# Optimization experiments

Hardware: AMD Instinct MI355X
Metric: run time of the kernel (lower is better)

The kernel has to match this reference:

```python
import jax, jax.numpy as jnp
import numpy as np

RADIUS = 0.2
NSAMPLE = 32
USE_XYZ = True

B, N, S, C = 8, 8192, 2048, 64


def setup_inputs() -> dict:
    key = jax.random.key(0)
    k1, k2, k3 = jax.random.split(key, 3)
    xyz = jax.random.uniform(k1, (B, N, 3), dtype=jnp.float32)
    new_xyz = jax.random.uniform(k2, (B, S, 3), dtype=jnp.float32)
    features = jax.random.normal(k3, (B, N, C), dtype=jnp.float32)
    return {"xyz": xyz, "new_xyz": new_xyz, "features": features}


def _ball_query(new_xyz, xyz, radius, nsample):
    # new_xyz: (B,S,3), xyz: (B,N,3) -> idx (B,S,nsample) int32
    n = xyz.shape[1]
    d2 = jnp.sum((new_xyz[:, :, None, :] - xyz[:, None, :, :]) ** 2, axis=-1)  # (B,S,N)
    mask = d2 < radius * radius
    # keys: index j if inside ball else N (sentinel); smallest nsample keys = first
    # nsample in-ball indices in ascending j order (matches CUDA ball_query order).
    keys = jnp.where(mask, jnp.arange(n, dtype=jnp.int32), jnp.int32(n))
    neg_vals, _ = jax.lax.top_k(-keys, nsample)  # top_k of -keys -> smallest keys
    idx = -neg_vals  # (B,S,nsample), ascending
    first = idx[..., 0:1]
    idx = jnp.where(idx == n, first, idx)   # pad empty slots with first hit
    idx = jnp.where(idx == n, 0, idx)       # balls with zero hits -> index 0
    return idx


def _group(points, idx):
    # points: (B,N,D), idx: (B,S,K) -> (B,S,K,D)
    return jax.vmap(lambda p, i: p[i])(points, idx)


def reference(xyz, new_xyz, features):
    idx = _ball_query(new_xyz, xyz, RADIUS, NSAMPLE)
    grouped_xyz = _group(xyz, idx) - new_xyz[:, :, None, :]  # (B,S,K,3)
    grouped_feat = _group(features, idx)                      # (B,S,K,C)
    if USE_XYZ:
        new_features = jnp.concatenate([grouped_xyz, grouped_feat], axis=-1)
    else:
        new_features = grouped_feat
    return jnp.transpose(new_features, (0, 3, 1, 2))  # (B, C+3, S, K)
```

## Files before the change

### kernel.cpp

```cpp
#include <hip/hip_runtime.h>

#define BB 8
#define NN 8192
#define SS 2048
#define CC 64
#define NS 32
#define COUT 67
#define QT 8
#define SLOTS (QT*NS)
#define SP 260

__global__ __launch_bounds__(256, 6) void fused_kernel(
    const float* __restrict__ xyz,
    const float* __restrict__ new_xyz,
    const float* __restrict__ feat,
    float* __restrict__ out)
{
#pragma clang fp contract(off)
    __shared__ float fh[16 * SP];
    __shared__ float xt[3 * SP];
    __shared__ int idx_sh[SLOTS];

    const int t   = threadIdx.x;
    const int w   = t >> 6;
    const int ln  = t & 63;
    const int bid = blockIdx.x;
    const int b     = bid & 7;
    const int sTile = bid >> 3;
    const int s0 = sTile * QT;

    for (int qi = 0; qi < 2; ++qi) {
        const int q = (qi << 2) + w;
        const int s = s0 + q;
        const float R2 = 0.04f;

        const float* ctr = new_xyz + ((size_t)b * SS + s) * 3;
        const float cx = ctr[0], cy = ctr[1], cz = ctr[2];
        const float* xb = xyz + (size_t)b * NN * 3;

        int* myidx = idx_sh + (q << 5);
        const unsigned long long lt = (1ull << ln) - 1ull;

        int total = 0;
        int firstIdx = -1;
        for (int j0 = 0; j0 < NN && total < NS; j0 += 256) {
            const float4* p4 = (const float4*)(xb + (size_t)(j0 + (ln << 2)) * 3);
            const float4 A  = p4[0];
            const float4 Bv = p4[1];
            const float4 Cv = p4[2];
            float d2v[4];
            {
                const float dx = A.x - cx, dy = A.y - cy, dz = A.z - cz;
                float d2 = dx * dx; d2 = d2 + dy * dy; d2 = d2 + dz * dz;
                d2v[0] = d2;
            }
            {
                const float dx = A.w - cx, dy = Bv.x - cy, dz = Bv.y - cz;
                float d2 = dx * dx; d2 = d2 + dy * dy; d2 = d2 + dz * dz;
                d2v[1] = d2;
            }
            {
                const float dx = Bv.z - cx, dy = Bv.w - cy, dz = Cv.x - cz;
                float d2 = dx * dx; d2 = d2 + dy * dy; d2 = d2 + dz * dz;
                d2v[2] = d2;
            }
            {
                const float dx = Cv.y - cx, dy = Cv.z - cy, dz = Cv.w - cz;
                float d2 = dx * dx; d2 = d2 + dy * dy; d2 = d2 + dz * dz;
                d2v[3] = d2;
            }

            unsigned long long M[4];
#pragma unroll
            for (int u = 0; u < 4; ++u) M[u] = __ballot(d2v[u] < R2);

            if (firstIdx < 0) {
                int fmin = 0x7fffffff;
#pragma unroll
                for (int u = 0; u < 4; ++u)
                    if (M[u] != 0ull) {
                        const int j = j0 + (__builtin_ctzll(M[u]) << 2) + u;
                        fmin = (j < fmin) ? j : fmin;
                    }
                if (fmin != 0x7fffffff) firstIdx = fmin;
            }

            int below = 0;
#pragma unroll
            for (int u = 0; u < 4; ++u) below += (int)__popcll(M[u] & lt);

            int own = 0;
#pragma unroll
            for (int u = 0; u < 4; ++u) {
                if (d2v[u] < R2) {
                    const int pos = total + below + own;
                    if (pos < NS) myidx[pos] = j0 + (ln << 2) + u;
                    ++own;
                }
            }
#pragma unroll
            for (int u = 0; u < 4; ++u) total += (int)__popcll(M[u]);
        }
        if (total < NS) {
            const int fill = (total > 0) ? firstIdx : 0;
            if (ln >= total && ln < NS) myidx[ln] = fill;
        }
    }
    __syncthreads();

    const int c4  = ln & 3;
    const int ms  = ln >> 2;
    const float* fb = feat + (size_t)b * NN * CC;
    const size_t plane = (size_t)SS * NS;
    float* ob = out + ((size_t)b * COUT * SS + s0) * NS;

    {
        const int r = idx_sh[t];
        const int q = t >> 5;
        const float* ctr = new_xyz + ((size_t)b * SS + s0 + q) * 3;
        const float* p   = xyz + ((size_t)b * NN + r) * 3;
        xt[0 * SP + t] = p[0] - ctr[0];
        xt[1 * SP + t] = p[1] - ctr[1];
        xt[2 * SP + t] = p[2] - ctr[2];
    }

#pragma unroll
    for (int st = 0; st < 4; ++st) {
        if (st > 0) __syncthreads();

        float4 vv[4];
        int    mm[4];
#pragma unroll
        for (int i = 0; i < 4; ++i) {
            mm[i] = (w << 6) + (i << 4) + ms;
            vv[i] = *(const float4*)(fb + (size_t)idx_sh[mm[i]] * CC
                                     + (st << 4) + (c4 << 2));
        }
#pragma unroll
        for (int i = 0; i < 4; ++i) {
            fh[((c4 << 2) + 0) * SP + mm[i]] = vv[i].x;
            fh[((c4 << 2) + 1) * SP + mm[i]] = vv[i].y;
            fh[((c4 << 2) + 2) * SP + mm[i]] = vv[i].z;
            fh[((c4 << 2) + 3) * SP + mm[i]] = vv[i].w;
        }
        __syncthreads();

        if (st == 0) {
            for (int i = 0; i < 5; ++i) {
                const int tau = (i << 2) + w;
                if (tau < 19) {
                    const float* src = (tau < 3) ? (xt + tau * SP)
                                                 : (fh + (tau - 3) * SP);
                    const float4 v = *(const float4*)(src + (ln << 2));
                    *(float4*)(ob + (size_t)tau * plane + (ln << 2)) = v;
                }
            }
        } else {
#pragma unroll
            for (int i = 0; i < 4; ++i) {
                const int tau = (i << 2) + w;
                const float4 v = *(const float4*)(fh + tau * SP + (ln << 2));
                *(float4*)(ob + (size_t)(3 + (st << 4) + tau) * plane
                           + (ln << 2)) = v;
            }
        }
    }
}

extern "C" void kernel_launch(void* const* d_in, const int* in_sizes, int n_in,
                              void* d_out, int out_size, void* d_ws, size_t ws_size,
                              hipStream_t stream) {
    const float* xyz     = (const float*)d_in[0];
    const float* new_xyz = (const float*)d_in[1];
    const float* feat    = (const float*)d_in[2];
    float* out = (float*)d_out;
    (void)d_ws; (void)ws_size;

    fused_kernel<<<dim3((BB * SS) / QT), dim3(256), 0, stream>>>(xyz, new_xyz, feat, out);
}
```

Measured before the change: 175.5 us.

## Software-pipeline feature gather in 8-channel stages with smaller shared tile

The feature gather now moves 8 channels per stage over 8 stages instead of 16 channels over 4. The next stage's global loads are issued before the barrier, so they overlap with the current stage's shared-to-global stores. The shared feature buffer is halved, and launch bounds now ask for 8 blocks per CU to raise occupancy. The cost is twice as many barriers and stages, each global load now fetching only 32 bytes per row (two lanes per gather row instead of four), and tighter register limits.

Result: no change. 177.0 us (+0.8%).

```diff
diff --git a/kernel.cpp b/kernel.cpp
--- a/kernel.cpp
+++ b/kernel.cpp
@@ -10,14 +10,14 @@
 #define SLOTS (QT*NS)
 #define SP 260
 
-__global__ __launch_bounds__(256, 6) void fused_kernel(
+__global__ __launch_bounds__(256, 8) void fused_kernel(
     const float* __restrict__ xyz,
     const float* __restrict__ new_xyz,
     const float* __restrict__ feat,
     float* __restrict__ out)
 {
 #pragma clang fp contract(off)
-    __shared__ float fh[16 * SP];
+    __shared__ float fh[8 * SP];
     __shared__ float xt[3 * SP];
     __shared__ int idx_sh[SLOTS];
 
@@ -108,8 +108,8 @@
     }
     __syncthreads();
 
-    const int c4  = ln & 3;
-    const int ms  = ln >> 2;
+    const int c2 = ln & 1;
+    const int ms = ln >> 1;
     const float* fb = feat + (size_t)b * NN * CC;
     const size_t plane = (size_t)SS * NS;
     float* ob = out + ((size_t)b * COUT * SS + s0) * NS;
@@ -124,31 +124,35 @@
         xt[2 * SP + t] = p[2] - ctr[2];
     }
 
+    const int m0 = (w << 6) + ms;
+    const int m1 = m0 + 32;
+    const float* rp0 = fb + (size_t)idx_sh[m0] * CC + (c2 << 2);
+    const float* rp1 = fb + (size_t)idx_sh[m1] * CC + (c2 << 2);
+
+    float4 v0 = *(const float4*)(rp0);
+    float4 v1 = *(const float4*)(rp1);
+
 #pragma unroll
-    for (int st = 0; st < 4; ++st) {
-        if (st > 0) __syncthreads();
+    for (int st = 0; st < 8; ++st) {
+        fh[((c2 << 2) + 0) * SP + m0] = v0.x;
+        fh[((c2 << 2) + 1) * SP + m0] = v0.y;
+        fh[((c2 << 2) + 2) * SP + m0] = v0.z;
+        fh[((c2 << 2) + 3) * SP + m0] = v0.w;
+        fh[((c2 << 2) + 0) * SP + m1] = v1.x;
+        fh[((c2 << 2) + 1) * SP + m1] = v1.y;
+        fh[((c2 << 2) + 2) * SP + m1] = v1.z;
+        fh[((c2 << 2) + 3) * SP + m1] = v1.w;
 
-        float4 vv[4];
-        int    mm[4];
-#pragma unroll
-        for (int i = 0; i < 4; ++i) {
-            mm[i] = (w << 6) + (i << 4) + ms;
-            vv[i] = *(const float4*)(fb + (size_t)idx_sh[mm[i]] * CC
-                                     + (st << 4) + (c4 << 2));
-        }
-#pragma unroll
-        for (int i = 0; i < 4; ++i) {
-            fh[((c4 << 2) + 0) * SP + mm[i]] = vv[i].x;
-            fh[((c4 << 2) + 1) * SP + mm[i]] = vv[i].y;
-            fh[((c4 << 2) + 2) * SP + mm[i]] = vv[i].z;
-            fh[((c4 << 2) + 3) * SP + mm[i]] = vv[i].w;
+        if (st < 7) {
+            v0 = *(const float4*)(rp0 + ((st + 1) << 3));
+            v1 = *(const float4*)(rp1 + ((st + 1) << 3));
         }
         __syncthreads();
 
         if (st == 0) {
-            for (int i = 0; i < 5; ++i) {
+            for (int i = 0; i < 3; ++i) {
                 const int tau = (i << 2) + w;
-                if (tau < 19) {
+                if (tau < 11) {
                     const float* src = (tau < 3) ? (xt + tau * SP)
                                                  : (fh + (tau - 3) * SP);
                     const float4 v = *(const float4*)(src + (ln << 2));
@@ -157,13 +161,14 @@
             }
         } else {
 #pragma unroll
-            for (int i = 0; i < 4; ++i) {
-                const int tau = (i << 2) + w;
-                const float4 v = *(const float4*)(fh + tau * SP + (ln << 2));
-                *(float4*)(ob + (size_t)(3 + (st << 4) + tau) * plane
+            for (int i = 0; i < 2; ++i) {
+                const int pl = (i << 2) + w;
+                const float4 v = *(const float4*)(fh + pl * SP + (ln << 2));
+                *(float4*)(ob + (size_t)(3 + (st << 3) + pl) * plane
                            + (ln << 2)) = v;
             }
         }
+        if (st < 7) __syncthreads();
     }
 }
 
```
